# Kernel tuning notes

Measured on AMD Instinct MI355X. Metric: run time of the kernel, lower is better.

## Reference

```python
import jax, jax.numpy as jnp
import numpy as np
from jax import lax

NEG = -1e30  # log-space 'zero' that stays finite for stable grads

T, B, V, L = 2000, 64, 128, 100


def ctc_cost(acts, labels2d, sizes, label_lens):
    """warp-ctc style CTC: acts are raw logits (T,B,V), blank index 0.
    Returns summed negative log-likelihood over the batch, shape (1,)."""
    Tn, Bn, Vn = acts.shape
    Ln = labels2d.shape[1]
    S = 2 * Ln + 1  # extended label length: blank,l1,blank,l2,...,blank
    lp = jax.nn.log_softmax(acts, axis=-1)  # (T,B,V)

    # extended label sequence per example: even positions blank(0), odd = labels
    ext = jnp.zeros((Bn, S), dtype=labels2d.dtype).at[:, 1::2].set(labels2d)
    # skip (s-2 -> s) allowed iff ext[s] != blank and ext[s] != ext[s-2]
    prev2 = jnp.concatenate([jnp.full((Bn, 2), -1, ext.dtype), ext[:, :-2]], axis=1)
    can_skip = (ext != 0) & (ext != prev2)  # (B,S)

    # gather per-state emission log-probs for all timesteps: (T,B,S)
    lp_ext = jnp.take_along_axis(lp, jnp.broadcast_to(ext[None], (Tn, Bn, S)), axis=2)

    # alpha init at t=0: states 0 (blank) and 1 (first label)
    alpha0 = (jnp.full((Bn, S), NEG, lp.dtype)
              .at[:, 0].set(lp_ext[0, :, 0])
              .at[:, 1].set(lp_ext[0, :, 1]))

    # per-timestep activity mask: freeze alpha once t >= sizes[b]
    active = jnp.arange(1, Tn)[:, None] < sizes[None, :]  # (T-1, B)

    def step(alpha, x):
        lp_t, act = x  # (B,S), (B,)
        a1 = jnp.concatenate([jnp.full((Bn, 1), NEG, alpha.dtype), alpha[:, :-1]], axis=1)
        a2 = jnp.concatenate([jnp.full((Bn, 2), NEG, alpha.dtype), alpha[:, :-2]], axis=1)
        a2 = jnp.where(can_skip, a2, NEG)
        new = jnp.logaddexp(jnp.logaddexp(alpha, a1), a2) + lp_t
        alpha = jnp.where(act[:, None], new, alpha)
        return alpha, None

    alpha, _ = lax.scan(step, alpha0, (lp_ext[1:], active))

    # log-likelihood ends at extended states S_b-1 (final blank) and S_b-2 (final label)
    S_b = 2 * label_lens + 1
    last = jnp.take_along_axis(alpha, (S_b - 1)[:, None], axis=1)[:, 0]
    last2 = jnp.take_along_axis(alpha, (S_b - 2)[:, None], axis=1)[:, 0]
    ll = jnp.logaddexp(last, last2)  # (B,)
    return -jnp.sum(ll)[None]  # shape (1,) like the torch module


def setup_inputs() -> dict:
    key = jax.random.key(0)
    k1, k2, k3 = jax.random.split(key, 3)
    inp = jax.random.normal(k1, (T, B, V), dtype=jnp.float32)
    # labels in [1, V): 0 is reserved for blank
    target = jax.random.randint(k2, (B * L,), 1, V, dtype=jnp.int32)
    # frame counts in [T//2, T], always >= 2L+1 so every path is feasible
    sizes = jax.random.randint(k3, (B,), T // 2, T + 1, dtype=jnp.int32)
    label_lens = jnp.full((B,), L, dtype=jnp.int32)
    return {"input": inp, "target": target, "sizes": sizes, "label_lens": label_lens}


def reference(input, target, sizes, label_lens):
    labels2d = target.reshape(sizes.shape[0], -1)  # all label_lens equal -> clean reshape
    return ctc_cost(input, labels2d, sizes, label_lens)
```

## Files before the change

### kernel.cpp

```cpp
#include <hip/hip_runtime.h>


#define TT 2000
#define BB 64
#define VV 128
#define LL 100
#define RECW 56
#define REC_BASE 256
#define NEGF (-1e30f)
#define L2E 1.44269504f
#define LN2 0.69314718f

#define SB_STATE (REC_BASE + BB * TT * RECW)
#define AREA 336

__device__ __forceinline__ float wave_max64(float v) {
#pragma unroll
  for (int o = 32; o > 0; o >>= 1) v = fmaxf(v, __shfl_xor(v, o, 64));
  return v;
}
__device__ __forceinline__ float wave_sum64(float v) {
#pragma unroll
  for (int o = 32; o > 0; o >>= 1) v += __shfl_xor(v, o, 64);
  return v;
}
__device__ __forceinline__ float blo(unsigned u) { return __uint_as_float(u << 16); }
__device__ __forceinline__ float bhi(unsigned u) { return __uint_as_float(u & 0xFFFF0000u); }
__device__ __forceinline__ unsigned b16(float x) {
  unsigned b = __float_as_uint(x);
  return (b + 0x7FFFu + ((b >> 16) & 1u)) >> 16;
}

__global__ __launch_bounds__(256) void k_gather(const float* __restrict__ acts,
                                                const int* __restrict__ target,
                                                float* __restrict__ ws) {
  const int lane = threadIdx.x & 63;
  const int w = threadIdx.x >> 6;
  const int r = blockIdx.x * 4 + w;
  if (r >= TT * BB) return;
  const int b = r % BB;
  const int t = r / BB;
  const float* row = acts + (size_t)r * VV;
  float x0 = row[lane];
  float x1 = row[lane + 64];
  float m = wave_max64(fmaxf(x0, x1));
  float e = __builtin_exp2f((x0 - m) * L2E) + __builtin_exp2f((x1 - m) * L2E);
  float s = wave_sum64(e);
  float lse = m + __builtin_log2f(s) * LN2;
  const int* lab = target + b * LL;
  const int j = lane;
  int ilo = (2 * j < 100) ? 2 * j : 99;
  int ihi = (2 * j + 1 < 100) ? 2 * j + 1 : 99;
  int cl = lab[ilo], ch = lab[ihi];
  float ya = __shfl(x0, cl & 63, 64), yb = __shfl(x1, cl & 63, 64);
  float ylo = (cl < 64) ? ya : yb;
  float yc = __shfl(x0, ch & 63, 64), yd = __shfl(x1, ch & 63, 64);
  float yhi = (ch < 64) ? yc : yd;
  float glo = (j < 50) ? (ylo - lse) : NEGF;
  float ghi = (j < 50) ? (yhi - lse) : NEGF;
  float gb = __shfl(x0, 0, 64) - lse;
  float gm = wave_max64(fmaxf(fmaxf(glo, ghi), gb));
  float qlo = __builtin_exp2f((glo - gm) * L2E);
  float qhi = __builtin_exp2f((ghi - gm) * L2E);
  unsigned u = b16(qlo) | (b16(qhi) << 16);
  unsigned* rec = (unsigned*)(ws + REC_BASE + ((size_t)b * TT + t) * RECW);
  if (j < 50) rec[2 + j] = u;
  if (j == 50) rec[52] = 0u;
  if (j == 0) {
    ((float*)rec)[0] = __builtin_exp2f((gb - gm) * L2E);
    ((float*)rec)[1] = gm;
  }
}

#define BPER __builtin_amdgcn_ds_bpermute
#define CL50(x) ((x) < 0 ? 0 : ((x) > 50 ? 50 : (x)))

#define DECLR(P) float2 P##h0, P##h1, P##h2, P##h3; \
                 unsigned P##b0, P##b1, P##b2, P##b3, P##c0, P##c1, P##c2, P##c3, P##uA

#define PREF(P, bidx) do {                                                   \
  int bi_ = (bidx); bi_ = (bi_ < bcap) ? bi_ : bcap; if (bi_ < 0) bi_ = 0;   \
  const float* r0_ = recs_b + (size_t)(tA + TS * 4 * bi_) * RECW;            \
  P##h0 = *(const float2*)(r0_);                                             \
  P##h1 = *(const float2*)(r0_ + TS * RECW);                                 \
  P##h2 = *(const float2*)(r0_ + TS * 2 * RECW);                             \
  P##h3 = *(const float2*)(r0_ + TS * 3 * RECW);                             \
  P##b0 = ((const unsigned*)r0_)[pbofs];                                     \
  P##c0 = ((const unsigned*)r0_)[pcofs];                                     \
  P##b1 = ((const unsigned*)(r0_ + TS * RECW))[pbofs];                       \
  P##c1 = ((const unsigned*)(r0_ + TS * RECW))[pcofs];                       \
  P##b2 = ((const unsigned*)(r0_ + TS * 2 * RECW))[pbofs];                   \
  P##c2 = ((const unsigned*)(r0_ + TS * 2 * RECW))[pcofs];                   \
  P##b3 = ((const unsigned*)(r0_ + TS * 3 * RECW))[pbofs];                   \
  P##c3 = ((const unsigned*)(r0_ + TS * 3 * RECW))[pcofs];                   \
  P##uA = ((const unsigned*)r0_)[payofs];                                    \
} while (0)

#define STEP(qbv, gmv, cx, cy, bx, by, ay, NH) do {                          \
  const float qb_ = (qbv); msum += (gmv);                                    \
  o3 = __builtin_fmaf(cs_o3, o1, o3 + o2) * (cy);                            \
  o2 = (o2 + o1) * qb_;                                                      \
  o1 = __builtin_fmaf(cs_o1, h1, o1 + o0) * (cx);                            \
  o0 = (o0 + h1) * qb_;                                                      \
  if (NH >= 1) { h1 = __builtin_fmaf(cs_h1, h3, h1 + h2) * (by);             \
                 h2 = (h2 + h3) * qb_; }                                     \
  if (NH >= 2) { h3 = __builtin_fmaf(cs_h3, h5, h3 + h4) * (bx);             \
                 h4 = (h4 + h5) * qb_; }                                     \
  if (NH >= 3) { h5 = __builtin_fmaf(cs_h5, h7, h5 + h6) * (ay);             \
                 h6 = (h6 + h7) * qb_; }                                     \
} while (0)

#define UQ(P, K, QV) float4 QV; do {                                         \
  if constexpr (DIR) {                                                       \
    QV = (float4){bhi(P##b##K), blo(P##b##K),                                \
                  bhi(P##c##K) * cmask, blo(P##c##K) * cmask};               \
  } else {                                                                   \
    QV = (float4){blo(P##b##K), bhi(P##b##K), blo(P##c##K), bhi(P##c##K)};   \
  }                                                                          \
} while (0)

#define COMPA(P) do {                                                        \
  UQ(P, 0, q0_); UQ(P, 1, q1_); UQ(P, 2, q2_); UQ(P, 3, q3_);                \
  float aYv = DIR ? blo(P##uA) : bhi(P##uA);                                 \
  STEP(P##h0.x, P##h0.y, q0_.z, q0_.w, q0_.x, q0_.y, aYv, 3);                \
  STEP(P##h1.x, P##h1.y, q1_.z, q1_.w, q1_.x, q1_.y, 0.f, 2);                \
  STEP(P##h2.x, P##h2.y, q2_.z, q2_.w, q2_.x, q2_.y, 0.f, 1);                \
  STEP(P##h3.x, P##h3.y, q3_.z, q3_.w, 0.f, 0.f, 0.f, 0);                    \
  *(float4*)(exb + 4 * l) = (float4){o0, o1, o2, o3};                        \
  ((int*)exb)[256 + l] = offs;                                               \
} while (0)

#define FINL() do {                                                          \
  asm volatile("" ::: "memory");                                             \
  float4 L1_ = *(const float4*)(exb + 4 * ((l >= 1) ? (l - 1) : 0));         \
  float4 L2_ = *(const float4*)(exb + 4 * ((l >= 2) ? (l - 2) : 0));         \
  int ro1_ = ((const int*)exb)[256 + ((l >= 1) ? (l - 1) : 0)];              \
  int ro2_ = ((const int*)exb)[256 + ((l >= 2) ? (l - 2) : 0)];              \
  ro1_ = (l >= 1) ? ro1_ : -(1 << 29);                                       \
  ro2_ = (l >= 2) ? ro2_ : -(1 << 29);                                       \
  float m_ = fmaxf(fmaxf(o0, o1), fmaxf(o2, o3));                            \
  int eb_ = (int)((__float_as_uint(m_) >> 23) & 255u);                       \
  int t1_ = offs + (eb_ ? (eb_ - 127) : -126);                               \
  int mx_ = (ro1_ > ro2_) ? ro1_ : ro2_;                                     \
  int onew_ = (t1_ > mx_) ? t1_ : mx_;                                       \
  int ds_ = offs - onew_;  ds_ = (ds_ < -300) ? -300 : ds_;                  \
  int d1_ = ro1_ - onew_, d2_ = ro2_ - onew_;                                \
  d1_ = (d1_ < -300) ? -300 : d1_;                                           \
  d2_ = (d2_ < -300) ? -300 : d2_;                                           \
  o0 = ldexpf(o0, ds_); o1 = ldexpf(o1, ds_);                                \
  o2 = ldexpf(o2, ds_); o3 = ldexpf(o3, ds_);                                \
  h1 = ldexpf(L1_.w, d1_) * msk1;                                            \
  h2 = ldexpf(L1_.z, d1_) * msk2;                                            \
  h3 = ldexpf(L1_.y, d1_) * msk3;                                            \
  h4 = ldexpf(L1_.x, d1_) * msk4;                                            \
  h5 = ldexpf(L2_.w, d2_) * msk5;                                            \
  h6 = ldexpf(L2_.z, d2_) * msk6;                                            \
  h7 = ldexpf(L2_.y, d2_) * msk7;                                            \
  offs = onew_;                                                              \
} while (0)

template <int DIR>
__device__ __forceinline__ void run_chain(const int* __restrict__ target,
                                          const int* __restrict__ lablens,
                                          const float* __restrict__ recs_b,
                                          float* exb, int size, int b, int l,
                                          float* __restrict__ ws) {
  const int mid = (size - 1) >> 1;
  const int sizeP = DIR ? (size - 1 - mid) : (mid + 1);
  const int* lab = target + b * LL;
  const int lc = (l < 50) ? l : 50;
  const int tA = DIR ? (size - 2) : 1;
  constexpr int TS = DIR ? -1 : 1;
  const int bcap = DIR ? ((size - 5) >> 2) : 498;
  const int pbofs = 2 + (DIR ? CL50(50 - l) : CL50(l - 1));
  const int pcofs = 2 + (DIR ? CL50(49 - l) : CL50(l));
  const int payofs = 2 + (DIR ? CL50(51 - l) : CL50(l - 2));
  const float cmask = (l < 50) ? 1.f : 0.f;
  const int idx1 = ((l + 63) & 63) << 2;
  const float msk1 = (4 * l - 1 >= 0) ? 1.f : 0.f;
  const float msk2 = (4 * l - 2 >= 0) ? 1.f : 0.f;
  const float msk3 = (4 * l - 3 >= 0) ? 1.f : 0.f;
  const float msk4 = (4 * l - 4 >= 0) ? 1.f : 0.f;
  const float msk5 = (4 * l - 5 >= 0) ? 1.f : 0.f;
  const float msk6 = (4 * l - 6 >= 0) ? 1.f : 0.f;
  const float msk7 = (4 * l - 7 >= 0) ? 1.f : 0.f;
  int i0, i1, i2, i3, i4, i5;
  if constexpr (DIR == 0) { i0 = 2*l+1; i1 = 2*l; i2 = 2*l-1; i3 = 2*l-2; i4 = 2*l-3; i5 = 2*l-4; }
  else { i0 = 98-2*l; i1 = 99-2*l; i2 = 100-2*l; i3 = 101-2*l; i4 = 102-2*l; i5 = 103-2*l; }
#define CLM(x) ((x) < 0 ? 0 : ((x) > 99 ? 99 : (x)))
  const int La = lab[CLM(i0)], Lb_ = lab[CLM(i1)], Lc = lab[CLM(i2)];
  const int Ld = lab[CLM(i3)], Le = lab[CLM(i4)], Lf = lab[CLM(i5)];
  const float cs_o3 = (La != Lb_) ? 1.f : 0.f;
  const float cs_o1 = (Lb_ != Lc) ? 1.f : 0.f;
  const float cs_h1 = (Lc != Ld) ? 1.f : 0.f;
  const float cs_h3 = (Ld != Le) ? 1.f : 0.f;
  const float cs_h5 = (Le != Lf) ? 1.f : 0.f;
  float o0 = 0.f, o1 = 0.f, o2 = 0.f, o3 = 0.f;
  float h1 = 0.f, h2 = 0.f, h3 = 0.f, h4 = 0.f, h5 = 0.f, h6 = 0.f, h7 = 0.f;
  int offs = 0;
  float msum;
  if constexpr (DIR == 0) {
    msum = recs_b[1];
    float q0i = blo(((const unsigned*)recs_b)[2]);
    if (l == 0) { o0 = recs_b[0]; o1 = q0i; }
    if (l == 1) { h3 = q0i; h4 = recs_b[0]; }
    if (l == 2) { h7 = q0i; }
  } else {
    const float* recL = recs_b + (size_t)(size - 1) * RECW;
    msum = recL[1];
    const int Lbv = lablens[b];
    const int r0v = 200 - 2 * Lbv;
    auto gi = [&](int rho) -> float {
      if (rho != r0v && rho != r0v + 1) return 0.f;
      if ((rho & 1) == 0) return recL[0];
      int mm = 99 - ((rho - 1) >> 1);
      unsigned u = ((const unsigned*)recL)[2 + (mm >> 1)];
      return (mm & 1) ? bhi(u) : blo(u);
    };
    o0 = gi(4*l); o1 = gi(4*l+1); o2 = gi(4*l+2); o3 = gi(4*l+3);
    h1 = gi(4*l-1); h2 = gi(4*l-2); h3 = gi(4*l-3); h4 = gi(4*l-4);
    h5 = gi(4*l-5); h6 = gi(4*l-6); h7 = gi(4*l-7);
  }

  const int nb = (sizeP - 1) >> 2;
  DECLR(A); DECLR(B); DECLR(C);
  PREF(A, 0); PREF(B, 1);
  int blk = 0;
  for (; blk + 3 <= nb; blk += 3) {
    COMPA(A); PREF(C, blk + 2); FINL();
    COMPA(B); PREF(A, blk + 3); FINL();
    COMPA(C); PREF(B, blk + 4); FINL();
  }
  if (nb - blk >= 1) { COMPA(A); FINL(); }
  if (nb - blk >= 2) { COMPA(B); FINL(); }
  {
    int rno1 = BPER(idx1, offs);
    int dtl = rno1 - offs;
    dtl = (dtl > 120) ? 120 : ((dtl < -300) ? -300 : dtl);
    for (int tau = 1 + 4 * nb; tau < sizeP; ++tau) {
      const float* rt = recs_b + (size_t)(DIR ? (size - 1 - tau) : tau) * RECW;
      float2 hh = *(const float2*)rt;
      float cx, cy;
      if constexpr (DIR == 0) {
        unsigned u = ((const unsigned*)rt)[2 + lc];
        cx = blo(u); cy = bhi(u);
      } else {
        unsigned u = ((const unsigned*)rt)[2 + CL50(50 - l)];
        cx = bhi(u) * cmask; cy = blo(u) * cmask;
      }
      int rp = BPER(idx1, __float_as_int(o3));
      float p = ldexpf(__int_as_float(rp), dtl) * msk1;
      msum += hh.y;
      o3 = __builtin_fmaf(cs_o3, o1, o3 + o2) * cy;
      o2 = (o2 + o1) * hh.x;
      o1 = __builtin_fmaf(cs_o1, p, o1 + o0) * cx;
      o0 = (o0 + p) * hh.x;
    }
    if constexpr (DIR == 0) {
      int rp = BPER(idx1, __float_as_int(o3));
      float p = ldexpf(__int_as_float(rp), dtl) * msk1;
      o3 = __builtin_fmaf(cs_o3, o1, o3 + o2);
      o2 = o2 + o1;
      o1 = __builtin_fmaf(cs_o1, p, o1 + o0);
      o0 = o0 + p;
    }
  }
  float* da = ws + SB_STATE + (size_t)(2 * b + DIR) * AREA;
  ((float4*)da)[l] = (float4){o0, o1, o2, o3};
  ((int*)da)[256 + l] = offs;
  if (l == 0) da[320] = msum;
}

__global__ __launch_bounds__(128, 1) void k_alpha(const int* __restrict__ target,
                                                  const int* __restrict__ sizes,
                                                  const int* __restrict__ lablens,
                                                  float* __restrict__ ws) {
  __shared__ float ldsA[2 * 384];
  const int b = blockIdx.x;
  const int dirw = threadIdx.x >> 6;
  const int l = threadIdx.x & 63;
  float* exb = ldsA + dirw * 384;
  const int size = sizes[b];
  const float* recs_b = ws + REC_BASE + (size_t)b * TT * RECW;
  if (dirw == 0) run_chain<0>(target, lablens, recs_b, exb, size, b, l, ws);
  else           run_chain<1>(target, lablens, recs_b, exb, size, b, l, ws);
}

__global__ __launch_bounds__(64) void k_comb(float* __restrict__ ws) {
  const int b = blockIdx.x;
  const int l = threadIdx.x;
  const float* fa = ws + SB_STATE + (size_t)(2 * b) * AREA;
  const float* ba = fa + AREA;
  float4 av = ((const float4*)fa)[l];
  int eF = ((const int*)fa)[256 + l];
  float msF = fa[320], msB = ba[320];
  float pr0, pr1, pr2, pr3; int ex0, ex1, ex2, ex3, sb0, sb1, sb2, sb3;
#define CMP(k, AV, PR, EX, SBE) do {                                         \
    int s_ = 4 * l + (k);                                                    \
    int rho_ = 200 - s_;                                                     \
    int rc_ = (rho_ < 0) ? 0 : rho_;                                         \
    float g_ = ba[rc_];                                                      \
    int eB_ = ((const int*)ba)[256 + (rc_ >> 2)];                            \
    float p_ = (AV) * g_;                                                    \
    bool ok_ = (rho_ >= 0) && (p_ > 0.f);                                    \
    int eb_ = (int)((__float_as_uint(p_) >> 23) & 255u);                     \
    SBE = eF + eB_;                                                          \
    EX = ok_ ? (SBE + (eb_ ? eb_ - 127 : -140)) : (int)0xC0000000;           \
    PR = ok_ ? p_ : 0.f;                                                     \
  } while (0)
  CMP(0, av.x, pr0, ex0, sb0);
  CMP(1, av.y, pr1, ex1, sb1);
  CMP(2, av.z, pr2, ex2, sb2);
  CMP(3, av.w, pr3, ex3, sb3);
  int Em = ex0 > ex1 ? ex0 : ex1;
  Em = ex2 > Em ? ex2 : Em;
  Em = ex3 > Em ? ex3 : Em;
#pragma unroll
  for (int o = 32; o > 0; o >>= 1) {
    int t = __shfl_xor(Em, o, 64);
    Em = (t > Em) ? t : Em;
  }
  float v = 0.f;
#define ACC(PR, SBE) do { if (PR > 0.f) {                                    \
    int sh_ = SBE - Em; sh_ = sh_ < -300 ? -300 : (sh_ > 300 ? 300 : sh_);   \
    v += ldexpf(PR, sh_); } } while (0)
  ACC(pr0, sb0); ACC(pr1, sb1); ACC(pr2, sb2); ACC(pr3, sb3);
  float S = wave_sum64(v);
  if (l == 0) ws[b] = msF + msB + LN2 * ((float)Em + __builtin_log2f(S));
}

__global__ __launch_bounds__(64) void k_final(const float* __restrict__ ws, float* __restrict__ out) {
  float v = (threadIdx.x < BB) ? ws[threadIdx.x] : 0.0f;
  v = wave_sum64(v);
  if (threadIdx.x == 0) out[0] = -v;
}

extern "C" void kernel_launch(void* const* d_in, const int* in_sizes, int n_in,
                              void* d_out, int out_size, void* d_ws, size_t ws_size,
                              hipStream_t stream) {
  const float* acts  = (const float*)d_in[0];
  const int* target  = (const int*)d_in[1];
  const int* sizes   = (const int*)d_in[2];
  const int* lablens = (const int*)d_in[3];
  float* ws  = (float*)d_ws;
  float* out = (float*)d_out;
  const int nrec = TT * BB;
  k_gather<<<dim3(nrec / 4), dim3(256), 0, stream>>>(acts, target, ws);
  k_alpha<<<dim3(BB), dim3(128), 0, stream>>>(target, sizes, lablens, ws);
  k_comb<<<dim3(BB), dim3(64), 0, stream>>>(ws);
  k_final<<<dim3(1), dim3(64), 0, stream>>>(ws, out);
}
```

Before: 124.5 us.

## Fuse forward/backward combine into alpha kernel and pack LDS exchange as bf16

New measurement: 125.2 us. Within noise of the previous version (+0.6%).

```diff
diff --git a/kernel.cpp b/kernel.cpp
--- a/kernel.cpp
+++ b/kernel.cpp
@@ -10,9 +10,6 @@
 #define NEGF (-1e30f)
 #define L2E 1.44269504f
 #define LN2 0.69314718f
-
-#define SB_STATE (REC_BASE + BB * TT * RECW)
-#define AREA 336
 
 __device__ __forceinline__ float wave_max64(float v) {
 #pragma unroll
@@ -126,16 +123,18 @@
   STEP(P##h1.x, P##h1.y, q1_.z, q1_.w, q1_.x, q1_.y, 0.f, 2);                \
   STEP(P##h2.x, P##h2.y, q2_.z, q2_.w, q2_.x, q2_.y, 0.f, 1);                \
   STEP(P##h3.x, P##h3.y, q3_.z, q3_.w, 0.f, 0.f, 0.f, 0);                    \
-  *(float4*)(exb + 4 * l) = (float4){o0, o1, o2, o3};                        \
-  ((int*)exb)[256 + l] = offs;                                               \
+  unsigned p01_ = b16(o0) | (b16(o1) << 16);                                 \
+  unsigned p23_ = b16(o2) | (b16(o3) << 16);                                 \
+  *(uint2*)(exbU + 2 * l) = (uint2){p01_, p23_};                             \
+  exbU[128 + l] = (unsigned)offs;                                            \
 } while (0)
 
 #define FINL() do {                                                          \
   asm volatile("" ::: "memory");                                             \
-  float4 L1_ = *(const float4*)(exb + 4 * ((l >= 1) ? (l - 1) : 0));         \
-  float4 L2_ = *(const float4*)(exb + 4 * ((l >= 2) ? (l - 2) : 0));         \
-  int ro1_ = ((const int*)exb)[256 + ((l >= 1) ? (l - 1) : 0)];              \
-  int ro2_ = ((const int*)exb)[256 + ((l >= 2) ? (l - 2) : 0)];              \
+  uint2 W1_ = *(const uint2*)(exbU + 2 * ((l >= 1) ? (l - 1) : 0));          \
+  uint2 W2_ = *(const uint2*)(exbU + 2 * ((l >= 2) ? (l - 2) : 0));          \
+  int ro1_ = (int)exbU[128 + ((l >= 1) ? (l - 1) : 0)];                      \
+  int ro2_ = (int)exbU[128 + ((l >= 2) ? (l - 2) : 0)];                      \
   ro1_ = (l >= 1) ? ro1_ : -(1 << 29);                                       \
   ro2_ = (l >= 2) ? ro2_ : -(1 << 29);                                       \
   float m_ = fmaxf(fmaxf(o0, o1), fmaxf(o2, o3));                            \
@@ -149,13 +148,13 @@
   d2_ = (d2_ < -300) ? -300 : d2_;                                           \
   o0 = ldexpf(o0, ds_); o1 = ldexpf(o1, ds_);                                \
   o2 = ldexpf(o2, ds_); o3 = ldexpf(o3, ds_);                                \
-  h1 = ldexpf(L1_.w, d1_) * msk1;                                            \
-  h2 = ldexpf(L1_.z, d1_) * msk2;                                            \
-  h3 = ldexpf(L1_.y, d1_) * msk3;                                            \
-  h4 = ldexpf(L1_.x, d1_) * msk4;                                            \
-  h5 = ldexpf(L2_.w, d2_) * msk5;                                            \
-  h6 = ldexpf(L2_.z, d2_) * msk6;                                            \
-  h7 = ldexpf(L2_.y, d2_) * msk7;                                            \
+  h1 = ldexpf(bhi(W1_.y), d1_);                                              \
+  h2 = ldexpf(blo(W1_.y), d1_);                                              \
+  h3 = ldexpf(bhi(W1_.x), d1_);                                              \
+  h4 = ldexpf(blo(W1_.x), d1_);                                              \
+  h5 = ldexpf(bhi(W2_.y), d2_);                                              \
+  h6 = ldexpf(blo(W2_.y), d2_);                                              \
+  h7 = ldexpf(bhi(W2_.x), d2_);                                              \
   offs = onew_;                                                              \
 } while (0)
 
@@ -163,8 +162,8 @@
 __device__ __forceinline__ void run_chain(const int* __restrict__ target,
                                           const int* __restrict__ lablens,
                                           const float* __restrict__ recs_b,
-                                          float* exb, int size, int b, int l,
-                                          float* __restrict__ ws) {
+                                          float* exb, int size, int b, int l) {
+  unsigned* exbU = (unsigned*)exb;
   const int mid = (size - 1) >> 1;
   const int sizeP = DIR ? (size - 1 - mid) : (mid + 1);
   const int* lab = target + b * LL;
@@ -178,12 +177,6 @@
   const float cmask = (l < 50) ? 1.f : 0.f;
   const int idx1 = ((l + 63) & 63) << 2;
   const float msk1 = (4 * l - 1 >= 0) ? 1.f : 0.f;
-  const float msk2 = (4 * l - 2 >= 0) ? 1.f : 0.f;
-  const float msk3 = (4 * l - 3 >= 0) ? 1.f : 0.f;
-  const float msk4 = (4 * l - 4 >= 0) ? 1.f : 0.f;
-  const float msk5 = (4 * l - 5 >= 0) ? 1.f : 0.f;
-  const float msk6 = (4 * l - 6 >= 0) ? 1.f : 0.f;
-  const float msk7 = (4 * l - 7 >= 0) ? 1.f : 0.f;
   int i0, i1, i2, i3, i4, i5;
   if constexpr (DIR == 0) { i0 = 2*l+1; i1 = 2*l; i2 = 2*l-1; i3 = 2*l-2; i4 = 2*l-3; i5 = 2*l-4; }
   else { i0 = 98-2*l; i1 = 99-2*l; i2 = 100-2*l; i3 = 101-2*l; i4 = 102-2*l; i5 = 103-2*l; }
@@ -265,10 +258,10 @@
       o0 = o0 + p;
     }
   }
-  float* da = ws + SB_STATE + (size_t)(2 * b + DIR) * AREA;
-  ((float4*)da)[l] = (float4){o0, o1, o2, o3};
-  ((int*)da)[256 + l] = offs;
-  if (l == 0) da[320] = msum;
+  asm volatile("" ::: "memory");
+  ((float4*)exb)[l] = (float4){o0, o1, o2, o3};
+  ((int*)exb)[256 + l] = offs;
+  if (l == 0) exb[320] = msum;
 }
 
 __global__ __launch_bounds__(128, 1) void k_alpha(const int* __restrict__ target,
@@ -282,51 +275,49 @@
   float* exb = ldsA + dirw * 384;
   const int size = sizes[b];
   const float* recs_b = ws + REC_BASE + (size_t)b * TT * RECW;
-  if (dirw == 0) run_chain<0>(target, lablens, recs_b, exb, size, b, l, ws);
-  else           run_chain<1>(target, lablens, recs_b, exb, size, b, l, ws);
-}
-
-__global__ __launch_bounds__(64) void k_comb(float* __restrict__ ws) {
-  const int b = blockIdx.x;
-  const int l = threadIdx.x;
-  const float* fa = ws + SB_STATE + (size_t)(2 * b) * AREA;
-  const float* ba = fa + AREA;
-  float4 av = ((const float4*)fa)[l];
-  int eF = ((const int*)fa)[256 + l];
-  float msF = fa[320], msB = ba[320];
-  float pr0, pr1, pr2, pr3; int ex0, ex1, ex2, ex3, sb0, sb1, sb2, sb3;
+  if (dirw == 0) run_chain<0>(target, lablens, recs_b, exb, size, b, l);
+  else           run_chain<1>(target, lablens, recs_b, exb, size, b, l);
+  __syncthreads();
+  if (dirw == 0) {
+    const float* fa = ldsA;
+    const float* ba = ldsA + 384;
+    float4 av = ((const float4*)fa)[l];
+    int eF = ((const int*)fa)[256 + l];
+    float msF = fa[320], msB = ba[320];
+    float pr0, pr1, pr2, pr3; int ex0, ex1, ex2, ex3, sb0, sb1, sb2, sb3;
 #define CMP(k, AV, PR, EX, SBE) do {                                         \
-    int s_ = 4 * l + (k);                                                    \
-    int rho_ = 200 - s_;                                                     \
-    int rc_ = (rho_ < 0) ? 0 : rho_;                                         \
-    float g_ = ba[rc_];                                                      \
-    int eB_ = ((const int*)ba)[256 + (rc_ >> 2)];                            \
-    float p_ = (AV) * g_;                                                    \
-    bool ok_ = (rho_ >= 0) && (p_ > 0.f);                                    \
-    int eb_ = (int)((__float_as_uint(p_) >> 23) & 255u);                     \
-    SBE = eF + eB_;                                                          \
-    EX = ok_ ? (SBE + (eb_ ? eb_ - 127 : -140)) : (int)0xC0000000;           \
-    PR = ok_ ? p_ : 0.f;                                                     \
-  } while (0)
-  CMP(0, av.x, pr0, ex0, sb0);
-  CMP(1, av.y, pr1, ex1, sb1);
-  CMP(2, av.z, pr2, ex2, sb2);
-  CMP(3, av.w, pr3, ex3, sb3);
-  int Em = ex0 > ex1 ? ex0 : ex1;
-  Em = ex2 > Em ? ex2 : Em;
-  Em = ex3 > Em ? ex3 : Em;
+      int s_ = 4 * l + (k);                                                  \
+      int rho_ = 200 - s_;                                                   \
+      int rc_ = (rho_ < 0) ? 0 : rho_;                                       \
+      float g_ = ba[rc_];                                                    \
+      int eB_ = ((const int*)ba)[256 + (rc_ >> 2)];                          \
+      float p_ = (AV) * g_;                                                  \
+      bool ok_ = (rho_ >= 0) && (p_ > 0.f);                                  \
+      int eb_ = (int)((__float_as_uint(p_) >> 23) & 255u);                   \
+      SBE = eF + eB_;                                                        \
+      EX = ok_ ? (SBE + (eb_ ? eb_ - 127 : -140)) : (int)0xC0000000;         \
+      PR = ok_ ? p_ : 0.f;                                                   \
+    } while (0)
+    CMP(0, av.x, pr0, ex0, sb0);
+    CMP(1, av.y, pr1, ex1, sb1);
+    CMP(2, av.z, pr2, ex2, sb2);
+    CMP(3, av.w, pr3, ex3, sb3);
+    int Em = ex0 > ex1 ? ex0 : ex1;
+    Em = ex2 > Em ? ex2 : Em;
+    Em = ex3 > Em ? ex3 : Em;
 #pragma unroll
-  for (int o = 32; o > 0; o >>= 1) {
-    int t = __shfl_xor(Em, o, 64);
-    Em = (t > Em) ? t : Em;
-  }
-  float v = 0.f;
+    for (int o = 32; o > 0; o >>= 1) {
+      int t = __shfl_xor(Em, o, 64);
+      Em = (t > Em) ? t : Em;
+    }
+    float v = 0.f;
 #define ACC(PR, SBE) do { if (PR > 0.f) {                                    \
-    int sh_ = SBE - Em; sh_ = sh_ < -300 ? -300 : (sh_ > 300 ? 300 : sh_);   \
-    v += ldexpf(PR, sh_); } } while (0)
-  ACC(pr0, sb0); ACC(pr1, sb1); ACC(pr2, sb2); ACC(pr3, sb3);
-  float S = wave_sum64(v);
-  if (l == 0) ws[b] = msF + msB + LN2 * ((float)Em + __builtin_log2f(S));
+      int sh_ = SBE - Em; sh_ = sh_ < -300 ? -300 : (sh_ > 300 ? 300 : sh_); \
+      v += ldexpf(PR, sh_); } } while (0)
+    ACC(pr0, sb0); ACC(pr1, sb1); ACC(pr2, sb2); ACC(pr3, sb3);
+    float S = wave_sum64(v);
+    if (l == 0) ws[b] = msF + msB + LN2 * ((float)Em + __builtin_log2f(S));
+  }
 }
 
 __global__ __launch_bounds__(64) void k_final(const float* __restrict__ ws, float* __restrict__ out) {
@@ -347,6 +338,5 @@
   const int nrec = TT * BB;
   k_gather<<<dim3(nrec / 4), dim3(256), 0, stream>>>(acts, target, ws);
   k_alpha<<<dim3(BB), dim3(128), 0, stream>>>(target, sizes, lablens, ws);
-  k_comb<<<dim3(BB), dim3(64), 0, stream>>>(ws);
   k_final<<<dim3(1), dim3(64), 0, stream>>>(ws, out);
 }
```
